# Performance work log

Hardware: AMD Instinct MI355X
Metric: run time of the kernel (lower is better)

Reference implementation:

```python
import jax, jax.numpy as jnp
import numpy as np

EPS = 1e-5
B, N, D, H = 4, 2048, 1024, 16
DH = D // H


def ln(x, w, b):
    m = x.mean(-1, keepdims=True)
    v = ((x - m) ** 2).mean(-1, keepdims=True)
    return (x - m) * jax.lax.rsqrt(v + EPS) * w + b


def setup_inputs() -> dict:
    key = jax.random.key(0)
    ks = jax.random.split(key, 12)
    s = D ** -0.5
    x = jax.random.normal(ks[0], (B, N, D), jnp.float32)
    attention_mask = jax.random.randint(ks[1], (B, N), 0, 2) > 0
    return {
        "x": x,
        "attention_mask": attention_mask,
        "norm_w": jnp.ones((D,), jnp.float32),
        "norm_b": jnp.zeros((D,), jnp.float32),
        "qn_w": jnp.ones((DH,), jnp.float32),
        "qn_b": jnp.zeros((DH,), jnp.float32),
        "kn_w": jnp.ones((DH,), jnp.float32),
        "kn_b": jnp.zeros((DH,), jnp.float32),
        "Wq": jax.random.normal(ks[2], (D, D), jnp.float32) * s,
        "bq": jnp.zeros((D,), jnp.float32),
        "Wk": jax.random.normal(ks[3], (D, D), jnp.float32) * s,
        "bk": jnp.zeros((D,), jnp.float32),
        "Wv": jax.random.normal(ks[4], (D, D), jnp.float32) * s,
        "bv": jnp.zeros((D,), jnp.float32),
        "Wo": jax.random.normal(ks[5], (D, D), jnp.float32) * s,
    }


def reference(x, attention_mask, norm_w, norm_b, qn_w, qn_b, kn_w, kn_b,
              Wq, bq, Wk, bk, Wv, bv, Wo):
    b, n, d = x.shape
    scale = DH ** -0.5
    xn = ln(x, norm_w, norm_b)                       # pre-norm; context = xn (self-attn)
    q = (xn @ Wq.T + bq).reshape(b, n, H, DH).transpose(0, 2, 1, 3)  # b h n d
    k = (xn @ Wk.T + bk).reshape(b, n, H, DH).transpose(0, 2, 1, 3)
    v = (xn @ Wv.T + bv).reshape(b, n, H, DH).transpose(0, 2, 1, 3)
    q = ln(q, qn_w, qn_b) * scale                    # QK layernorm over head dim
    k = ln(k, kn_w, kn_b)
    sim = jnp.einsum('bhid,bhjd->bhij', q, k)        # full [b,h,n,n] scores
    sim = jnp.where(attention_mask[:, None, None, :], sim, -jnp.inf)
    attn = jax.nn.softmax(sim, axis=-1)
    out = jnp.einsum('bhij,bhjd->bhid', attn, v)
    out = out.transpose(0, 2, 1, 3).reshape(b, n, d)
    return out @ Wo.T
```

## Files before the change

kernel.cpp:

```cpp
#include <hip/hip_runtime.h>
#include <hip/hip_bf16.h>
#include <cstdint>

typedef unsigned short u16;
typedef unsigned int   u32;
typedef __attribute__((ext_vector_type(8))) short short8;
typedef __attribute__((ext_vector_type(4))) float f32x4;
typedef __attribute__((ext_vector_type(4))) u32  u32x4;
typedef __attribute__((ext_vector_type(2))) u32  u32x2;

#define DEV static __device__ __forceinline__

DEV float bf2f(u16 u){ u32 t = ((u32)u) << 16; float f; __builtin_memcpy(&f, &t, 4); return f; }
DEV u16 f2bf(float f){ u32 t; __builtin_memcpy(&t, &f, 4); return (u16)((t + 0x7fffu + ((t >> 16) & 1u)) >> 16); }

#if __has_builtin(__builtin_amdgcn_exp2f)
DEV float fast_exp2(float x){ return __builtin_amdgcn_exp2f(x); }
#else
DEV float fast_exp2(float x){ return exp2f(x); }
#endif

DEV u32 pack_trunc(float x, float y){
    u32 tx, ty; __builtin_memcpy(&tx, &x, 4); __builtin_memcpy(&ty, &y, 4);
#if __has_builtin(__builtin_amdgcn_perm)
    return __builtin_amdgcn_perm(ty, tx, 0x07060302);
#else
    return (tx >> 16) | (ty & 0xFFFF0000u);
#endif
}

DEV void gload_lds16(const void* g, void* l) {
    __builtin_amdgcn_global_load_lds((__attribute__((address_space(1))) void*)(g),
                                     (__attribute__((address_space(3))) void*)(l), 16, 0, 0);
}

DEV short8 xchg_quads(u32 a0, u32 a1, u32 b0, u32 b1)
{
    u32 x0 = a0, y0 = b0;
    asm("v_permlane32_swap_b32 %0, %1" : "+v"(x0), "+v"(y0));
    asm("v_permlane16_swap_b32 %0, %1" : "+v"(x0), "+v"(y0));
    u32 x1 = a1, y1 = b1;
    asm("v_permlane32_swap_b32 %0, %1" : "+v"(x1), "+v"(y1));
    asm("v_permlane16_swap_b32 %0, %1" : "+v"(x1), "+v"(y1));
    union { u32 w[4]; short8 v; } u;
    u.w[0] = x0; u.w[1] = x1; u.w[2] = y0; u.w[3] = y1;
    return u.v;
}

__global__ __launch_bounds__(256) void detect_mode(const u16* __restrict__ x, int* __restrict__ mode)
{
    __shared__ int red[4];
    const int tid = threadIdx.x;
    int crazy = 0;
    for (int i = tid; i < 1024; i += 256) {
        u16 v = x[2 * i];
        int e = (v >> 7) & 0xFF;
        if (e >= 0x9F || (e > 0 && e <= 0x5F)) crazy++;
    }
    #pragma unroll
    for (int off = 1; off < 64; off <<= 1) crazy += __shfl_xor(crazy, off, 64);
    if ((tid & 63) == 0) red[tid >> 6] = crazy;
    __syncthreads();
    if (tid == 0) *mode = (red[0] + red[1] + red[2] + red[3] > 128) ? 1 : 0;
}

struct SrcPtrs { const void* p[13]; };

__global__ __launch_bounds__(256) void convert_params(SrcPtrs sp, u16* __restrict__ ws,
                                                      const int* __restrict__ mode)
{
    const bool f = (*mode != 0);
    u16* cW = ws + 33554432;
    u16* cV = ws + 37748736;
    if (blockIdx.x < 16384) {
        const int i = blockIdx.x * 256 + threadIdx.x;
        const int t = i >> 20, off = i & 1048575;
        const void* src = (t == 0) ? sp.p[6] : (t == 1) ? sp.p[8] : (t == 2) ? sp.p[10] : sp.p[12];
        cW[i] = f ? f2bf(((const float*)src)[off]) : ((const u16*)src)[off];
    } else {
        const int j = (blockIdx.x - 16384) * 256 + threadIdx.x;
        if (j >= 5376) return;
        const void* src; int off;
        if      (j < 1024) { src = sp.p[0];  off = j; }
        else if (j < 2048) { src = sp.p[1];  off = j - 1024; }
        else if (j < 3072) { src = sp.p[7];  off = j - 2048; }
        else if (j < 4096) { src = sp.p[9];  off = j - 3072; }
        else if (j < 5120) { src = sp.p[11]; off = j - 4096; }
        else { int m = j - 5120; src = sp.p[2 + (m >> 6)]; off = m & 63; }
        cV[j] = f ? f2bf(((const float*)src)[off]) : ((const u16*)src)[off];
    }
}

__global__ __launch_bounds__(256) void ln_kernel(const void* __restrict__ x,
                                                 const u16* __restrict__ w,
                                                 const u16* __restrict__ b,
                                                 u16* __restrict__ xn,
                                                 const int* __restrict__ mode)
{
    const int row = blockIdx.x;
    const int tid = threadIdx.x;
    const int wv = tid >> 6, lane = tid & 63;

    float v0, v1, v2, v3;
    if (*mode) {
        f32x4 r = *((const f32x4*)((const float*)x + row * 1024) + tid);
        v0 = r[0]; v1 = r[1]; v2 = r[2]; v3 = r[3];
    } else {
        u32x2 raw = *(const u32x2*)((const u16*)x + row * 1024 + tid * 4);
        v0 = bf2f((u16)(raw.x & 0xffff)); v1 = bf2f((u16)(raw.x >> 16));
        v2 = bf2f((u16)(raw.y & 0xffff)); v3 = bf2f((u16)(raw.y >> 16));
    }
    float s  = v0 + v1 + v2 + v3;
    float sq = v0*v0 + v1*v1 + v2*v2 + v3*v3;
    #pragma unroll
    for (int off = 1; off < 64; off <<= 1) {
        s  += __shfl_xor(s,  off, 64);
        sq += __shfl_xor(sq, off, 64);
    }
    __shared__ float red[8];
    if (lane == 0) { red[wv] = s; red[4 + wv] = sq; }
    __syncthreads();
    float ts = red[0] + red[1] + red[2] + red[3];
    float tq = red[4] + red[5] + red[6] + red[7];
    float mean = ts * (1.0f / 1024.0f);
    float var  = tq * (1.0f / 1024.0f) - mean * mean;
    float rs   = rsqrtf(var + 1e-5f);

    float y0 = (v0 - mean) * rs * bf2f(w[tid*4+0]) + bf2f(b[tid*4+0]);
    float y1 = (v1 - mean) * rs * bf2f(w[tid*4+1]) + bf2f(b[tid*4+1]);
    float y2 = (v2 - mean) * rs * bf2f(w[tid*4+2]) + bf2f(b[tid*4+2]);
    float y3 = (v3 - mean) * rs * bf2f(w[tid*4+3]) + bf2f(b[tid*4+3]);
    u32x2 out;
    out.x = (u32)f2bf(y0) | ((u32)f2bf(y1) << 16);
    out.y = (u32)f2bf(y2) | ((u32)f2bf(y3) << 16);
    *(u32x2*)(xn + row * 1024 + tid * 4) = out;
}

__global__ __launch_bounds__(256, 4) void gemm128(const u16* __restrict__ A,
                                                  const u16* __restrict__ W,
                                                  const u16* __restrict__ bias,
                                                  void* __restrict__ out0,
                                                  u16* __restrict__ vt,
                                                  const u16* __restrict__ qnw, const u16* __restrict__ qnb,
                                                  const u16* __restrict__ knw, const u16* __restrict__ knb,
                                                  const int* __restrict__ mode,
                                                  int epi, int N)
{
    __shared__ u16 As[128 * 64];
    __shared__ u16 Bs[128 * 64];
    const int tid = threadIdx.x;
    const int m0 = blockIdx.x * 128, n0 = blockIdx.y * 128;
    const int wv = tid >> 6, lane = tid & 63, quad = lane >> 4, l16 = lane & 15;
    const int wm = wv & 1, wn = wv >> 1;

    f32x4 acc[4][4] = {};

    const int srow = tid >> 3;
    const int scol = (((tid & 7) - (srow & 7)) & 7) * 8;
    const u16* Ap = A + (size_t)(m0 + srow) * 1024 + scol;
    const u16* Wp = W + (size_t)(n0 + srow) * 1024 + scol;

    const int swz0 = ((quad     + l16) & 7) * 8;
    const int swz1 = ((quad + 4 + l16) & 7) * 8;

    for (int k0 = 0; k0 < 1024; k0 += 64) {
        #pragma unroll
        for (int i = 0; i < 4; i++)
            gload_lds16(Ap + k0 + (size_t)i * 32 * 1024, &As[i * 2048 + wv * 512]);
        #pragma unroll
        for (int i = 0; i < 4; i++)
            gload_lds16(Wp + k0 + (size_t)i * 32 * 1024, &Bs[i * 2048 + wv * 512]);
        __syncthreads();
        #pragma unroll
        for (int kh = 0; kh < 2; kh++) {
            const int sw = kh ? swz1 : swz0;
            short8 af[4], bf[4];
            #pragma unroll
            for (int mi = 0; mi < 4; mi++)
                af[mi] = *(const short8*)&As[(wm * 64 + mi * 16 + l16) * 64 + sw];
            #pragma unroll
            for (int ni = 0; ni < 4; ni++)
                bf[ni] = *(const short8*)&Bs[(wn * 64 + ni * 16 + l16) * 64 + sw];
            #pragma unroll
            for (int mi = 0; mi < 4; mi++)
                #pragma unroll
                for (int ni = 0; ni < 4; ni++)
                    acc[mi][ni] = __builtin_amdgcn_mfma_f32_16x16x32_bf16(af[mi], bf[ni], acc[mi][ni], 0, 0, 0);
        }
        __syncthreads();
    }

    if (epi == 1) {
        const int colbase = n0 + wn * 64;
        if (colbase < 2048) {
            const bool isK = colbase >= 1024;
            const u16* lw = isK ? knw : qnw;
            const u16* lb = isK ? knb : qnb;
            const float scale = isK ? 1.0f : 0.18033688011112042f;
            float lnw[4], lnb2[4], bv[4];
            #pragma unroll
            for (int ni = 0; ni < 4; ni++) {
                const int dh = ni * 16 + l16;
                lnw[ni] = bf2f(lw[dh]); lnb2[ni] = bf2f(lb[dh]); bv[ni] = bf2f(bias[colbase + dh]);
            }
            u16* qk = (u16*)out0;
            #pragma unroll
            for (int mi = 0; mi < 4; mi++) {
                #pragma unroll
                for (int r = 0; r < 4; r++) {
                    float v[4];
                    float s = 0.0f, sq = 0.0f;
                    #pragma unroll
                    for (int ni = 0; ni < 4; ni++) {
                        v[ni] = acc[mi][ni][r] + bv[ni];
                        s += v[ni]; sq += v[ni] * v[ni];
                    }
                    #pragma unroll
                    for (int off = 1; off < 16; off <<= 1) {
                        s  += __shfl_xor(s,  off, 64);
                        sq += __shfl_xor(sq, off, 64);
                    }
                    const float mean = s * (1.0f / 64.0f);
                    const float var  = sq * (1.0f / 64.0f) - mean * mean;
                    const float rs   = rsqrtf(var + 1e-5f);
                    const int row = m0 + wm * 64 + mi * 16 + quad * 4 + r;
                    #pragma unroll
                    for (int ni = 0; ni < 4; ni++)
                        qk[(size_t)row * 2048 + colbase + ni * 16 + l16] =
                            f2bf(((v[ni] - mean) * rs * lnw[ni] + lnb2[ni]) * scale);
                }
            }
        } else {
            const int cp0 = colbase - 2048;
            #pragma unroll
            for (int ni = 0; ni < 4; ni++) {
                const int cp = cp0 + ni * 16 + l16;
                const int h = cp >> 6, dh = cp & 63;
                const float bvv = bf2f(bias[2048 + cp]);
                #pragma unroll
                for (int mi = 0; mi < 4; mi++) {
                    const int row0 = m0 + wm * 64 + mi * 16 + quad * 4;
                    const int bb = row0 >> 11, nn = row0 & 2047;
                    u32x2 pk;
                    pk.x = (u32)f2bf(acc[mi][ni][0] + bvv) | ((u32)f2bf(acc[mi][ni][1] + bvv) << 16);
                    pk.y = (u32)f2bf(acc[mi][ni][2] + bvv) | ((u32)f2bf(acc[mi][ni][3] + bvv) << 16);
                    *(u32x2*)&vt[(size_t)(((bb * 16 + h) * 64) + dh) * 2048 + nn] = pk;
                }
            }
        }
    } else {
        const bool f32o = (*mode != 0);
        #pragma unroll
        for (int ni = 0; ni < 4; ni++) {
            const int col = n0 + wn * 64 + ni * 16 + l16;
            #pragma unroll
            for (int mi = 0; mi < 4; mi++) {
                const int row0 = m0 + wm * 64 + mi * 16 + quad * 4;
                #pragma unroll
                for (int r = 0; r < 4; r++) {
                    const float val = acc[mi][ni][r];
                    if (f32o) ((float*)out0)[(size_t)(row0 + r) * 1024 + col] = val;
                    else      ((u16*)out0)[(size_t)(row0 + r) * 1024 + col]  = f2bf(val);
                }
            }
        }
    }
}

#define ATTN_STAGE(BUF) do { \
    gload_lds16(kp0, &Ks[BUF][wv * 1024]); \
    gload_lds16(kp1, &Ks[BUF][wv * 1024 + 512]); \
    gload_lds16(vp0, &Vs[BUF][wv * 1024]); \
    gload_lds16(vp1, &Vs[BUF][wv * 1024 + 512]); \
    kp0 += 64 * 2048; kp1 += 64 * 2048; vp0 += 64; vp1 += 64; } while (0)

#define ATTN_BODY(CUR, NXT, J0, DO_STAGE, DO_BAR) do { \
    if (DO_STAGE) ATTN_STAGE(NXT); \
    f32x4 sfr[2][4]; \
    _Pragma("unroll") \
    for (int sub = 0; sub < 4; sub++) { \
        short8 kf0 = *(const short8*)&Ks[CUR][krow + swz0 + sub * 1024]; \
        short8 kf1 = *(const short8*)&Ks[CUR][krow + swz1 + sub * 1024]; \
        f32x4 mrow = *(const f32x4*)&maskf[(J0) + sub * 16 + quad * 4]; \
        _Pragma("unroll") \
        for (int g = 0; g < 2; g++) { \
            f32x4 sz = mrow; \
            sz = __builtin_amdgcn_mfma_f32_16x16x32_bf16(kf0, qf[g][0], sz, 0, 0, 0); \
            sz = __builtin_amdgcn_mfma_f32_16x16x32_bf16(kf1, qf[g][1], sz, 0, 0, 0); \
            sfr[g][sub] = sz; \
        } \
    } \
    short8 pf[2][2]; \
    _Pragma("unroll") \
    for (int g = 0; g < 2; g++) { \
        float lp = 0.0f; \
        _Pragma("unroll") \
        for (int sub = 0; sub < 4; sub++) \
            _Pragma("unroll") \
            for (int r = 0; r < 4; r++) { \
                float e = fast_exp2(sfr[g][sub][r]); \
                sfr[g][sub][r] = e; lp += e; \
            } \
        l_lane[g] += lp; \
        u32 W00 = pack_trunc(sfr[g][0][0], sfr[g][0][1]); \
        u32 W01 = pack_trunc(sfr[g][0][2], sfr[g][0][3]); \
        u32 W10 = pack_trunc(sfr[g][1][0], sfr[g][1][1]); \
        u32 W11 = pack_trunc(sfr[g][1][2], sfr[g][1][3]); \
        u32 W20 = pack_trunc(sfr[g][2][0], sfr[g][2][1]); \
        u32 W21 = pack_trunc(sfr[g][2][2], sfr[g][2][3]); \
        u32 W30 = pack_trunc(sfr[g][3][0], sfr[g][3][1]); \
        u32 W31 = pack_trunc(sfr[g][3][2], sfr[g][3][3]); \
        pf[g][0] = xchg_quads(W00, W01, W10, W11); \
        pf[g][1] = xchg_quads(W20, W21, W30, W31); \
    } \
    _Pragma("unroll") \
    for (int dht = 0; dht < 4; dht++) { \
        short8 vf0 = *(const short8*)&Vs[CUR][krow + swz0 + dht * 1024]; \
        short8 vf1 = *(const short8*)&Vs[CUR][krow + swz1 + dht * 1024]; \
        _Pragma("unroll") \
        for (int g = 0; g < 2; g++) { \
            O[g][dht] = __builtin_amdgcn_mfma_f32_16x16x32_bf16(vf0, pf[g][0], O[g][dht], 0, 0, 0); \
            O[g][dht] = __builtin_amdgcn_mfma_f32_16x16x32_bf16(vf1, pf[g][1], O[g][dht], 0, 0, 0); \
        } \
    } \
    if (DO_BAR) { \
        asm volatile("s_waitcnt vmcnt(0)" ::: "memory"); \
        __builtin_amdgcn_s_barrier(); \
    } } while (0)

__global__ __launch_bounds__(256, 4) void attn(const u16* __restrict__ qk, const u16* __restrict__ vt,
                                               const int* __restrict__ mask, u16* __restrict__ ctx)
{
    __shared__ __align__(16) float maskf[2048];
    __shared__ __align__(16) u16 Ks[2][64 * 64];
    __shared__ __align__(16) u16 Vs[2][64 * 64];

    const int bh = blockIdx.y, b = bh >> 4, h = bh & 15;
    const int i0 = blockIdx.x * 128;
    const int tid = threadIdx.x, wv = tid >> 6, lane = tid & 63, quad = lane >> 4, l16 = lane & 15;

    for (int idx = tid; idx < 2048; idx += 256)
        maskf[idx] = mask[b * 2048 + idx] ? -12.0f : -1e9f;

    const u16* qbase = qk + (size_t)(b * 2048) * 2048 + h * 64;
    const u16* kbase = qbase + 1024;
    const u16* vbase = vt + (size_t)(bh * 64) * 2048;

    short8 qf[2][2];
    #pragma unroll
    for (int g = 0; g < 2; g++) {
        const int iw = i0 + wv * 32 + g * 16 + l16;
        qf[g][0] = *(const short8*)(qbase + (size_t)iw * 2048 + quad * 8);
        qf[g][1] = *(const short8*)(qbase + (size_t)iw * 2048 + 32 + quad * 8);
    }

    f32x4 O[2][4] = {};
    float l_lane[2] = {0.0f, 0.0f};

    const int sr = lane >> 3, ss = lane & 7;
    const int sck = ((ss - sr) & 7) * 8;
    const u16* kp0 = kbase + (size_t)(wv * 16 +      sr) * 2048 + sck;
    const u16* kp1 = kbase + (size_t)(wv * 16 + 8  + sr) * 2048 + sck;
    const u16* vp0 = vbase + (size_t)(wv * 16 +      sr) * 2048 + sck;
    const u16* vp1 = vbase + (size_t)(wv * 16 + 8  + sr) * 2048 + sck;

    const int swz0 = ((quad     + l16) & 7) * 8;
    const int swz1 = ((quad + 4 + l16) & 7) * 8;
    const int krow = l16 * 64;

    ATTN_STAGE(0);
    asm volatile("s_waitcnt vmcnt(0) lgkmcnt(0)" ::: "memory");
    __builtin_amdgcn_s_barrier();

    for (int j0 = 0; j0 < 2048; j0 += 128) {
        ATTN_BODY(0, 1, j0, true, true);
        const bool more = (j0 + 128) < 2048;
        ATTN_BODY(1, 0, j0 + 64, more, more);
    }

    #pragma unroll
    for (int g = 0; g < 2; g++) {
        float l = l_lane[g];
        l += __shfl_xor(l, 16, 64);
        l += __shfl_xor(l, 32, 64);
        const float inv = l > 0.0f ? 1.0f / l : 0.0f;
        const int iw = i0 + wv * 32 + g * 16 + l16;
        u16* cb = ctx + (size_t)(b * 2048 + iw) * 1024 + h * 64;
        #pragma unroll
        for (int dht = 0; dht < 4; dht++) {
            u32x2 pk;
            pk.x = (u32)f2bf(O[g][dht][0] * inv) | ((u32)f2bf(O[g][dht][1] * inv) << 16);
            pk.y = (u32)f2bf(O[g][dht][2] * inv) | ((u32)f2bf(O[g][dht][3] * inv) << 16);
            *(u32x2*)(cb + dht * 16 + quad * 4) = pk;
        }
    }
}

extern "C" void kernel_launch(void* const* d_in, const int* in_sizes, int n_in,
                              void* d_out, int out_size, void* d_ws, size_t ws_size,
                              hipStream_t stream)
{
    const int* mask = (const int*)d_in[1];

    u16* ws = (u16*)d_ws;
    u16* xn  = ws;
    u16* qkb = ws + 8388608;
    u16* vtb = ws + 25165824;
    u16* ctx = xn;
    u16* cW  = ws + 33554432;
    u16* cV  = ws + 37748736;
    int* mode = (int*)(ws + 37754176);

    detect_mode<<<dim3(1), dim3(256), 0, stream>>>((const u16*)d_in[0], mode);

    SrcPtrs sp;
    for (int i = 0; i < 13; i++) sp.p[i] = d_in[i + 2];
    convert_params<<<dim3(16405), dim3(256), 0, stream>>>(sp, ws, mode);

    ln_kernel<<<dim3(8192), dim3(256), 0, stream>>>(d_in[0], cV + 0, cV + 1024, xn, mode);

    gemm128<<<dim3(64, 24), dim3(256), 0, stream>>>(xn, cW, cV + 2048, qkb, vtb,
                                                    cV + 5120, cV + 5184, cV + 5248, cV + 5312,
                                                    mode, 1, 3072);

    attn<<<dim3(16, 64), dim3(256), 0, stream>>>(qkb, vtb, mask, ctx);

    gemm128<<<dim3(64, 8), dim3(256), 0, stream>>>(ctx, cW + 3145728, nullptr, d_out, nullptr,
                                                   nullptr, nullptr, nullptr, nullptr,
                                                   mode, 2, 1024);
}
```

Measured before the change: 297.8 us.

## Add double-buffered 128x256 QKV GEMM kernel and setprio around MFMA phases

After: 320.4 us. 1.08x slower.

```diff
diff --git a/kernel.cpp b/kernel.cpp
--- a/kernel.cpp
+++ b/kernel.cpp
@@ -138,13 +138,8 @@
 
 __global__ __launch_bounds__(256, 4) void gemm128(const u16* __restrict__ A,
                                                   const u16* __restrict__ W,
-                                                  const u16* __restrict__ bias,
                                                   void* __restrict__ out0,
-                                                  u16* __restrict__ vt,
-                                                  const u16* __restrict__ qnw, const u16* __restrict__ qnb,
-                                                  const u16* __restrict__ knw, const u16* __restrict__ knb,
-                                                  const int* __restrict__ mode,
-                                                  int epi, int N)
+                                                  const int* __restrict__ mode)
 {
     __shared__ u16 As[128 * 64];
     __shared__ u16 Bs[128 * 64];
@@ -190,78 +185,170 @@
         __syncthreads();
     }
 
-    if (epi == 1) {
-        const int colbase = n0 + wn * 64;
-        if (colbase < 2048) {
-            const bool isK = colbase >= 1024;
-            const u16* lw = isK ? knw : qnw;
-            const u16* lb = isK ? knb : qnb;
-            const float scale = isK ? 1.0f : 0.18033688011112042f;
-            float lnw[4], lnb2[4], bv[4];
-            #pragma unroll
-            for (int ni = 0; ni < 4; ni++) {
-                const int dh = ni * 16 + l16;
-                lnw[ni] = bf2f(lw[dh]); lnb2[ni] = bf2f(lb[dh]); bv[ni] = bf2f(bias[colbase + dh]);
+    const bool f32o = (*mode != 0);
+    #pragma unroll
+    for (int ni = 0; ni < 4; ni++) {
+        const int col = n0 + wn * 64 + ni * 16 + l16;
+        #pragma unroll
+        for (int mi = 0; mi < 4; mi++) {
+            const int row0 = m0 + wm * 64 + mi * 16 + quad * 4;
+            #pragma unroll
+            for (int r = 0; r < 4; r++) {
+                const float val = acc[mi][ni][r];
+                if (f32o) ((float*)out0)[(size_t)(row0 + r) * 1024 + col] = val;
+                else      ((u16*)out0)[(size_t)(row0 + r) * 1024 + col]  = f2bf(val);
             }
-            u16* qk = (u16*)out0;
-            #pragma unroll
-            for (int mi = 0; mi < 4; mi++) {
+        }
+    }
+}
+
+__global__ __launch_bounds__(512, 2) void gemm_qkv(const u16* __restrict__ A,
+                                                   const u16* __restrict__ W,
+                                                   const u16* __restrict__ bias,
+                                                   u16* __restrict__ qk,
+                                                   u16* __restrict__ vt,
+                                                   const u16* __restrict__ qnw, const u16* __restrict__ qnb,
+                                                   const u16* __restrict__ knw, const u16* __restrict__ knb)
+{
+    __shared__ u16 As[2][128 * 64];
+    __shared__ u16 Bs[2][256 * 64];
+    const int tid = threadIdx.x;
+    const int m0 = blockIdx.x * 128, n0 = blockIdx.y * 256;
+    const int wv = tid >> 6, lane = tid & 63, quad = lane >> 4, l16 = lane & 15;
+    const int wm = wv & 1, wn = wv >> 1;
+
+    f32x4 acc[4][4] = {};
+
+    const int srow = tid >> 3;
+    const int scol = (((tid & 7) - (srow & 7)) & 7) * 8;
+    const u16* Ap = A + (size_t)(m0 + srow) * 1024 + scol;
+    const u16* Wp = W + (size_t)(n0 + srow) * 1024 + scol;
+
+    const int swz0 = ((quad     + l16) & 7) * 8;
+    const int swz1 = ((quad + 4 + l16) & 7) * 8;
+
+#define STAGE_QKV(BUF, K) do { \
+    gload_lds16(Ap + (K) * 64,          &As[BUF][        wv * 512]); \
+    gload_lds16(Ap + (K) * 64 +  65536, &As[BUF][ 4096 + wv * 512]); \
+    gload_lds16(Wp + (K) * 64,          &Bs[BUF][        wv * 512]); \
+    gload_lds16(Wp + (K) * 64 +  65536, &Bs[BUF][ 4096 + wv * 512]); \
+    gload_lds16(Wp + (K) * 64 + 131072, &Bs[BUF][ 8192 + wv * 512]); \
+    gload_lds16(Wp + (K) * 64 + 196608, &Bs[BUF][12288 + wv * 512]); \
+} while (0)
+
+    STAGE_QKV(0, 0);
+    int cur = 0;
+    for (int t = 0; t < 16; ++t) {
+        asm volatile("s_waitcnt vmcnt(0)\n\ts_barrier" ::: "memory");
+        if (t < 15) STAGE_QKV(cur ^ 1, t + 1);
+
+        short8 af[4], bf[2];
+        #pragma unroll
+        for (int mi = 0; mi < 4; mi++)
+            af[mi] = *(const short8*)&As[cur][(wm * 64 + mi * 16 + l16) * 64 + swz0];
+        #pragma unroll
+        for (int ni = 0; ni < 2; ni++)
+            bf[ni] = *(const short8*)&Bs[cur][(wn * 64 + ni * 16 + l16) * 64 + swz0];
+        __builtin_amdgcn_s_setprio(1);
+        #pragma unroll
+        for (int mi = 0; mi < 4; mi++)
+            #pragma unroll
+            for (int ni = 0; ni < 2; ni++)
+                acc[mi][ni] = __builtin_amdgcn_mfma_f32_16x16x32_bf16(af[mi], bf[ni], acc[mi][ni], 0, 0, 0);
+        __builtin_amdgcn_s_setprio(0);
+        __builtin_amdgcn_s_barrier();
+        #pragma unroll
+        for (int ni = 0; ni < 2; ni++)
+            bf[ni] = *(const short8*)&Bs[cur][(wn * 64 + (2 + ni) * 16 + l16) * 64 + swz0];
+        __builtin_amdgcn_s_setprio(1);
+        #pragma unroll
+        for (int mi = 0; mi < 4; mi++)
+            #pragma unroll
+            for (int ni = 0; ni < 2; ni++)
+                acc[mi][2 + ni] = __builtin_amdgcn_mfma_f32_16x16x32_bf16(af[mi], bf[ni], acc[mi][2 + ni], 0, 0, 0);
+        __builtin_amdgcn_s_setprio(0);
+        __builtin_amdgcn_s_barrier();
+        #pragma unroll
+        for (int mi = 0; mi < 4; mi++)
+            af[mi] = *(const short8*)&As[cur][(wm * 64 + mi * 16 + l16) * 64 + swz1];
+        #pragma unroll
+        for (int ni = 0; ni < 2; ni++)
+            bf[ni] = *(const short8*)&Bs[cur][(wn * 64 + ni * 16 + l16) * 64 + swz1];
+        __builtin_amdgcn_s_setprio(1);
+        #pragma unroll
+        for (int mi = 0; mi < 4; mi++)
+            #pragma unroll
+            for (int ni = 0; ni < 2; ni++)
+                acc[mi][ni] = __builtin_amdgcn_mfma_f32_16x16x32_bf16(af[mi], bf[ni], acc[mi][ni], 0, 0, 0);
+        __builtin_amdgcn_s_setprio(0);
+        __builtin_amdgcn_s_barrier();
+        #pragma unroll
+        for (int ni = 0; ni < 2; ni++)
+            bf[ni] = *(const short8*)&Bs[cur][(wn * 64 + (2 + ni) * 16 + l16) * 64 + swz1];
+        __builtin_amdgcn_s_setprio(1);
+        #pragma unroll
+        for (int mi = 0; mi < 4; mi++)
+            #pragma unroll
+            for (int ni = 0; ni < 2; ni++)
+                acc[mi][2 + ni] = __builtin_amdgcn_mfma_f32_16x16x32_bf16(af[mi], bf[ni], acc[mi][2 + ni], 0, 0, 0);
+        __builtin_amdgcn_s_setprio(0);
+        cur ^= 1;
+    }
+#undef STAGE_QKV
+
+    const int colbase = n0 + wn * 64;
+    if (colbase < 2048) {
+        const bool isK = colbase >= 1024;
+        const u16* lw = isK ? knw : qnw;
+        const u16* lb = isK ? knb : qnb;
+        const float scale = isK ? 1.0f : 0.18033688011112042f;
+        float lnw[4], lnb2[4], bv[4];
+        #pragma unroll
+        for (int ni = 0; ni < 4; ni++) {
+            const int dh = ni * 16 + l16;
+            lnw[ni] = bf2f(lw[dh]); lnb2[ni] = bf2f(lb[dh]); bv[ni] = bf2f(bias[colbase + dh]);
+        }
+        #pragma unroll
+        for (int mi = 0; mi < 4; mi++) {
+            #pragma unroll
+            for (int r = 0; r < 4; r++) {
+                float v[4];
+                float s = 0.0f, sq = 0.0f;
                 #pragma unroll
-                for (int r = 0; r < 4; r++) {
-                    float v[4];
-                    float s = 0.0f, sq = 0.0f;
-                    #pragma unroll
-                    for (int ni = 0; ni < 4; ni++) {
-                        v[ni] = acc[mi][ni][r] + bv[ni];
-                        s += v[ni]; sq += v[ni] * v[ni];
-                    }
-                    #pragma unroll
-                    for (int off = 1; off < 16; off <<= 1) {
-                        s  += __shfl_xor(s,  off, 64);
-                        sq += __shfl_xor(sq, off, 64);
-                    }
-                    const float mean = s * (1.0f / 64.0f);
-                    const float var  = sq * (1.0f / 64.0f) - mean * mean;
-                    const float rs   = rsqrtf(var + 1e-5f);
-                    const int row = m0 + wm * 64 + mi * 16 + quad * 4 + r;
-                    #pragma unroll
-                    for (int ni = 0; ni < 4; ni++)
-                        qk[(size_t)row * 2048 + colbase + ni * 16 + l16] =
-                            f2bf(((v[ni] - mean) * rs * lnw[ni] + lnb2[ni]) * scale);
+                for (int ni = 0; ni < 4; ni++) {
+                    v[ni] = acc[mi][ni][r] + bv[ni];
+                    s += v[ni]; sq += v[ni] * v[ni];
                 }
-            }
-        } else {
-            const int cp0 = colbase - 2048;
-            #pragma unroll
-            for (int ni = 0; ni < 4; ni++) {
-                const int cp = cp0 + ni * 16 + l16;
-                const int h = cp >> 6, dh = cp & 63;
-                const float bvv = bf2f(bias[2048 + cp]);
                 #pragma unroll
-                for (int mi = 0; mi < 4; mi++) {
-                    const int row0 = m0 + wm * 64 + mi * 16 + quad * 4;
-                    const int bb = row0 >> 11, nn = row0 & 2047;
-                    u32x2 pk;
-                    pk.x = (u32)f2bf(acc[mi][ni][0] + bvv) | ((u32)f2bf(acc[mi][ni][1] + bvv) << 16);
-                    pk.y = (u32)f2bf(acc[mi][ni][2] + bvv) | ((u32)f2bf(acc[mi][ni][3] + bvv) << 16);
-                    *(u32x2*)&vt[(size_t)(((bb * 16 + h) * 64) + dh) * 2048 + nn] = pk;
+                for (int off = 1; off < 16; off <<= 1) {
+                    s  += __shfl_xor(s,  off, 64);
+                    sq += __shfl_xor(sq, off, 64);
                 }
+                const float mean = s * (1.0f / 64.0f);
+                const float var  = sq * (1.0f / 64.0f) - mean * mean;
+                const float rs   = rsqrtf(var + 1e-5f);
+                const int row = m0 + wm * 64 + mi * 16 + quad * 4 + r;
+                #pragma unroll
+                for (int ni = 0; ni < 4; ni++)
+                    qk[(size_t)row * 2048 + colbase + ni * 16 + l16] =
+                        f2bf(((v[ni] - mean) * rs * lnw[ni] + lnb2[ni]) * scale);
             }
         }
     } else {
-        const bool f32o = (*mode != 0);
+        const int cp0 = colbase - 2048;
         #pragma unroll
         for (int ni = 0; ni < 4; ni++) {
-            const int col = n0 + wn * 64 + ni * 16 + l16;
+            const int cp = cp0 + ni * 16 + l16;
+            const int h = cp >> 6, dh = cp & 63;
+            const float bvv = bf2f(bias[2048 + cp]);
             #pragma unroll
             for (int mi = 0; mi < 4; mi++) {
                 const int row0 = m0 + wm * 64 + mi * 16 + quad * 4;
-                #pragma unroll
-                for (int r = 0; r < 4; r++) {
-                    const float val = acc[mi][ni][r];
-                    if (f32o) ((float*)out0)[(size_t)(row0 + r) * 1024 + col] = val;
-                    else      ((u16*)out0)[(size_t)(row0 + r) * 1024 + col]  = f2bf(val);
-                }
+                const int bb = row0 >> 11, nn = row0 & 2047;
+                u32x2 pk;
+                pk.x = (u32)f2bf(acc[mi][ni][0] + bvv) | ((u32)f2bf(acc[mi][ni][1] + bvv) << 16);
+                pk.y = (u32)f2bf(acc[mi][ni][2] + bvv) | ((u32)f2bf(acc[mi][ni][3] + bvv) << 16);
+                *(u32x2*)&vt[(size_t)(((bb * 16 + h) * 64) + dh) * 2048 + nn] = pk;
             }
         }
     }
@@ -277,6 +364,7 @@
 #define ATTN_BODY(CUR, NXT, J0, DO_STAGE, DO_BAR) do { \
     if (DO_STAGE) ATTN_STAGE(NXT); \
     f32x4 sfr[2][4]; \
+    __builtin_amdgcn_s_setprio(1); \
     _Pragma("unroll") \
     for (int sub = 0; sub < 4; sub++) { \
         short8 kf0 = *(const short8*)&Ks[CUR][krow + swz0 + sub * 1024]; \
@@ -290,6 +378,7 @@
             sfr[g][sub] = sz; \
         } \
     } \
+    __builtin_amdgcn_s_setprio(0); \
     short8 pf[2][2]; \
     _Pragma("unroll") \
     for (int g = 0; g < 2; g++) { \
@@ -313,6 +402,7 @@
         pf[g][0] = xchg_quads(W00, W01, W10, W11); \
         pf[g][1] = xchg_quads(W20, W21, W30, W31); \
     } \
+    __builtin_amdgcn_s_setprio(1); \
     _Pragma("unroll") \
     for (int dht = 0; dht < 4; dht++) { \
         short8 vf0 = *(const short8*)&Vs[CUR][krow + swz0 + dht * 1024]; \
@@ -323,9 +413,9 @@
             O[g][dht] = __builtin_amdgcn_mfma_f32_16x16x32_bf16(vf1, pf[g][1], O[g][dht], 0, 0, 0); \
         } \
     } \
+    __builtin_amdgcn_s_setprio(0); \
     if (DO_BAR) { \
-        asm volatile("s_waitcnt vmcnt(0)" ::: "memory"); \
-        __builtin_amdgcn_s_barrier(); \
+        asm volatile("s_waitcnt vmcnt(0)\n\ts_barrier" ::: "memory"); \
     } } while (0)
 
 __global__ __launch_bounds__(256, 4) void attn(const u16* __restrict__ qk, const u16* __restrict__ vt,
@@ -369,8 +459,7 @@
     const int krow = l16 * 64;
 
     ATTN_STAGE(0);
-    asm volatile("s_waitcnt vmcnt(0) lgkmcnt(0)" ::: "memory");
-    __builtin_amdgcn_s_barrier();
+    asm volatile("s_waitcnt vmcnt(0) lgkmcnt(0)\n\ts_barrier" ::: "memory");
 
     for (int j0 = 0; j0 < 2048; j0 += 128) {
         ATTN_BODY(0, 1, j0, true, true);
@@ -419,13 +508,10 @@
 
     ln_kernel<<<dim3(8192), dim3(256), 0, stream>>>(d_in[0], cV + 0, cV + 1024, xn, mode);
 
-    gemm128<<<dim3(64, 24), dim3(256), 0, stream>>>(xn, cW, cV + 2048, qkb, vtb,
-                                                    cV + 5120, cV + 5184, cV + 5248, cV + 5312,
-                                                    mode, 1, 3072);
+    gemm_qkv<<<dim3(64, 12), dim3(512), 0, stream>>>(xn, cW, cV + 2048, qkb, vtb,
+                                                     cV + 5120, cV + 5184, cV + 5248, cV + 5312);
 
     attn<<<dim3(16, 64), dim3(256), 0, stream>>>(qkb, vtb, mask, ctx);
 
-    gemm128<<<dim3(64, 8), dim3(256), 0, stream>>>(ctx, cW + 3145728, nullptr, d_out, nullptr,
-                                                   nullptr, nullptr, nullptr, nullptr,
-                                                   mode, 2, 1024);
-}
+    gemm128<<<dim3(64, 8), dim3(256), 0, stream>>>(ctx, cW + 3145728, d_out, mode);
+}
```
